# Kernel tuning notes

Hardware: AMD Instinct MI355X
Metric: run time of the kernel (lower is better)

## Reference

```python
import jax, jax.numpy as jnp
import numpy as np


def setup_inputs() -> dict:
    key = jax.random.key(0)
    hidden_states = jax.random.normal(key, (8, 4096, 768), dtype=jnp.float32)
    return {"hidden_states": hidden_states}


def reference(hidden_states) -> jnp.ndarray:
    # fft along seq dim (-2), then along hidden dim (-1), keep real part.
    # Equivalent to a 2D FFT over the last two axes.
    x = hidden_states.astype(jnp.float32)
    out = jnp.fft.fft(jnp.fft.fft(x, axis=-2), axis=-1).real
    return out.astype(hidden_states.dtype)
```

## Files before the change

kernel.cpp:

```cpp
#include <hip/hip_runtime.h>
#include <hip/hip_bf16.h>

#define N1 4096
#define N2 768
#define NCC 384
#define CG 64
#define WS_NEEDED 100663296ull

__device__ __forceinline__ float2 cadd(float2 a, float2 b){ return make_float2(a.x+b.x, a.y+b.y); }
__device__ __forceinline__ float2 csub(float2 a, float2 b){ return make_float2(a.x-b.x, a.y-b.y); }
__device__ __forceinline__ float2 cmul(float2 a, float2 b){ return make_float2(a.x*b.x - a.y*b.y, a.x*b.y + a.y*b.x); }
__device__ __forceinline__ float2 cnegi(float2 a){ return make_float2(a.y, -a.x); }

__device__ __forceinline__ int rev6(int p) {
  int k = 0;
  #pragma unroll
  for (int i = 0; i < 6; ++i) { k = (k << 2) | (p & 3); p >>= 2; }
  return k;
}

__device__ __forceinline__ void fft8(float2 z[8]) {
  const float RH = 0.70710678118654752f;
  float2 u0=cadd(z[0],z[4]), v0=csub(z[0],z[4]);
  float2 u1=cadd(z[1],z[5]), v1=csub(z[1],z[5]);
  float2 u2=cadd(z[2],z[6]), v2=csub(z[2],z[6]);
  float2 u3=cadd(z[3],z[7]), v3=csub(z[3],z[7]);
  v1 = make_float2(RH*(v1.x+v1.y), RH*(v1.y-v1.x));
  v2 = cnegi(v2);
  v3 = make_float2(RH*(v3.y-v3.x), -RH*(v3.x+v3.y));
  float2 a0=cadd(u0,u2), b0=csub(u0,u2);
  float2 a1=cadd(u1,u3), b1=cnegi(csub(u1,u3));
  float2 c0=cadd(v0,v2), d0=csub(v0,v2);
  float2 c1=cadd(v1,v3), d1=cnegi(csub(v1,v3));
  z[0]=cadd(a0,a1); z[4]=csub(a0,a1);
  z[2]=cadd(b0,b1); z[6]=csub(b0,b1);
  z[1]=cadd(c0,c1); z[5]=csub(c0,c1);
  z[3]=cadd(d0,d1); z[7]=csub(d0,d1);
}

__global__ __launch_bounds__(1024) void p1a_kernel(const float* __restrict__ x,
                                                   float2* __restrict__ ws) {
  __shared__ float4 S4[64*65];
  float2* S = reinterpret_cast<float2*>(S4);
  int bid = blockIdx.x;
  int b8  = bid & 7;
  int rem = bid >> 3;
  int cg  = rem / 64;
  int a   = rem % 64;
  const int t = threadIdx.x, l = t & 63, w = t >> 6;

  const float* src = x + (size_t)b8 * N1 * N2 + (size_t)cg * 256;
  #pragma unroll
  for (int j = 0; j < 4; ++j) {
    int r   = 4*w + j;
    int row = a + 64*r;
    float4 v = *reinterpret_cast<const float4*>(src + (size_t)row * N2 + 4*l);
    S4[r*65 + l] = v;
  }
  __syncthreads();

  const int c = t & 127, b0 = t >> 7;
  float2 z[8];
  #pragma unroll
  for (int b1 = 0; b1 < 8; ++b1) z[b1] = S[(8*b1 + b0)*130 + c];
  fft8(z);
  {
    float sn, cs; __sincosf(-6.283185307179586f/64.f * (float)b0, &sn, &cs);
    float2 wstep = make_float2(cs, sn), wcur = wstep;
    #pragma unroll
    for (int j = 1; j < 8; ++j) { z[j] = cmul(z[j], wcur); wcur = cmul(wcur, wstep); }
  }
  __syncthreads();
  #pragma unroll
  for (int j = 0; j < 8; ++j) S[(j*8 + b0)*130 + c] = z[j];
  __syncthreads();

  const int jj = t >> 7;
  #pragma unroll
  for (int b0i = 0; b0i < 8; ++b0i) z[b0i] = S[(jj*8 + b0i)*130 + c];
  fft8(z);
  float2 wc, w8;
  { float sn, cs; __sincosf(-6.283185307179586f/4096.f * (float)(a*jj), &sn, &cs); wc = make_float2(cs, sn); }
  { float sn, cs; __sincosf(-6.283185307179586f/4096.f * (float)(8*a),  &sn, &cs); w8 = make_float2(cs, sn); }
  float2* wdst = ws + ((size_t)b8*64)*64*NCC + (size_t)a*NCC + cg*128 + c;
  #pragma unroll
  for (int m = 0; m < 8; ++m) {
    int kb = 8*m + jj;
    wdst[(size_t)kb * 64 * NCC] = cmul(z[m], wc);
    wc = cmul(wc, w8);
  }
}

__global__ __launch_bounds__(1024) void p1b_kernel(const float2* __restrict__ ws,
                                                   float* __restrict__ out) {
  __shared__ float2 T[2][4096];
  int bid = blockIdx.x;
  int b8  = bid & 7;
  int rem = bid >> 3;
  int cg  = rem / 32, kbt = rem % 32;
  int kb0 = (kbt == 0) ? 0  : kbt;
  int kb1 = (kbt == 0) ? 32 : 64 - kbt;
  const int t = threadIdx.x, l = t & 63, wv = (t >> 6) & 7, ti = t >> 9;
  const int kb = ti ? kb1 : kb0;

  const float2* wsrc = ws + (((size_t)b8*64 + kb)*64)*NCC + cg*CG + l;
  float2 z[8];
  #pragma unroll
  for (int a1 = 0; a1 < 8; ++a1)
    z[a1] = wsrc[(size_t)(8*a1 + wv) * NCC];
  fft8(z);
  float fac = -6.283185307179586f/64.0f * (float)wv;
  #pragma unroll
  for (int q = 1; q < 8; ++q) {
    float sn, cs; __sincosf(fac * (float)q, &sn, &cs);
    z[q] = cmul(z[q], make_float2(cs, sn));
  }
  #pragma unroll
  for (int q = 0; q < 8; ++q) T[ti][(q*8 + wv)*64 + l] = z[q];
  __syncthreads();
  #pragma unroll
  for (int a0 = 0; a0 < 8; ++a0) z[a0] = T[ti][(wv*8 + a0)*64 + l];
  fft8(z);
  __syncthreads();
  #pragma unroll
  for (int ka1 = 0; ka1 < 8; ++ka1) T[ti][(8*ka1 + wv)*64 + l] = z[ka1];
  __syncthreads();

  const size_t obase = (size_t)b8 * N1 * N2;
  #pragma unroll
  for (int it = 0; it < 8; ++it) {
    int ka = 8*it + wv;
    int tj, kap;
    if (kbt == 0) { tj = ti; kap = ti ? (63 - ka) : ((64 - ka) & 63); }
    else          { tj = 1 - ti; kap = 63 - ka; }
    float2 Zk = T[ti][ka*64 + l];
    float2 Zp = T[tj][kap*64 + l];
    int r = kb + 64*ka;
    float2 o;
    if (r <= 2048) o = make_float2(0.5f*(Zk.x + Zp.x), 0.5f*(Zk.y + Zp.y));
    else           o = make_float2(0.5f*(Zp.y - Zk.y), 0.5f*(Zk.x - Zp.x));
    *reinterpret_cast<float2*>(out + obase + (size_t)r * N2 + 2*(cg*CG + l)) = o;
  }
}

#define PADI(i) ((i) + ((i) >> 4))
#define CPBUF 4352

__device__ __forceinline__ void bfly4p(float2* arr, int base, int M, float fac, int np) {
  float2 a0 = arr[PADI(base)], a1 = arr[PADI(base+M)];
  float2 a2 = arr[PADI(base+2*M)], a3 = arr[PADI(base+3*M)];
  float2 t0 = cadd(a0,a2), t1 = csub(a0,a2);
  float2 t2 = cadd(a1,a3), t3 = cnegi(csub(a1,a3));
  float2 y0 = cadd(t0,t2), y1 = cadd(t1,t3), y2 = csub(t0,t2), y3 = csub(t1,t3);
  float ang = fac * (float)np;
  float sn, cs; __sincosf(ang, &sn, &cs);
  float2 w1 = make_float2(cs, sn);
  float2 w2 = cmul(w1,w1);
  float2 w3 = cmul(w2,w1);
  arr[PADI(base)]     = y0;
  arr[PADI(base+M)]   = cmul(y1,w1);
  arr[PADI(base+2*M)] = cmul(y2,w2);
  arr[PADI(base+3*M)] = cmul(y3,w3);
}

__global__ __launch_bounds__(1024) void fft_seq_fused(const float* __restrict__ x,
                                                      float* __restrict__ out) {
  extern __shared__ float2 lds[];
  int bid = blockIdx.x;
  int wg  = (bid & 7) * 96 + (bid >> 3);
  int b   = wg / 96;
  int g   = wg % 96;
  const int t = threadIdx.x;
  const size_t base = (size_t)b * N1 * N2 + 8 * (size_t)g;

  for (int r = t; r < N1; r += 1024) {
    const float* p = x + base + (size_t)r * N2;
    float4 A  = *reinterpret_cast<const float4*>(p);
    float4 Bv = *reinterpret_cast<const float4*>(p + 4);
    int ip = PADI(r);
    lds[ip]             = make_float2(A.x, A.y);
    lds[CPBUF + ip]     = make_float2(A.z, A.w);
    lds[2*CPBUF + ip]   = make_float2(Bv.x, Bv.y);
    lds[3*CPBUF + ip]   = make_float2(Bv.z, Bv.w);
  }
  __syncthreads();

  const int wv  = t >> 6;
  const int cp  = wv & 3;
  const int idx = ((wv >> 2) << 6) + (t & 63);
  float2* buf = lds + cp * CPBUF;

  #pragma unroll
  for (int s = 0; s < 6; ++s) {
    int lm = 10 - 2*s;
    int M  = 1 << lm;
    float fac = -6.283185307179586f / (float)(4*M);
    #pragma unroll
    for (int jj = 0; jj < 4; ++jj) {
      int j   = idx + (jj << 8);
      int np  = j & (M-1);
      int grp = j >> lm;
      int bse = (grp << (lm+2)) + np;
      bfly4p(buf, bse, M, fac, np);
    }
    __syncthreads();
  }

  float* orow = out + base;
  #pragma unroll
  for (int i = 0; i < 4; ++i) {
    int k  = ((t & 63) << 6) + (t >> 6) + (i << 4);
    int km = (N1 - k) & (N1 - 1);
    int pk = PADI(rev6(k));
    int pn = PADI(rev6(km));
    float o[8];
    #pragma unroll
    for (int c = 0; c < 4; ++c) {
      float2 zk = lds[c*CPBUF + pk];
      float2 zn = lds[c*CPBUF + pn];
      if (k <= 2048) { o[2*c] = 0.5f*(zk.x + zn.x); o[2*c+1] = 0.5f*(zk.y + zn.y); }
      else           { o[2*c] = 0.5f*(zn.y - zk.y); o[2*c+1] = 0.5f*(zk.x - zn.x); }
    }
    float* q = orow + (size_t)k * N2;
    *reinterpret_cast<float4*>(q)     = make_float4(o[0], o[1], o[2], o[3]);
    *reinterpret_cast<float4*>(q + 4) = make_float4(o[4], o[5], o[6], o[7]);
  }
}

__global__ __launch_bounds__(256) void fft_hid_kernel(float* __restrict__ out) {
  __shared__ float T[4][12*69];
  const int grp = threadIdx.x >> 6;
  const int l   = threadIdx.x & 63;
  int task = blockIdx.x * 4 + grp;
  int b  = task / 2049;
  int t1 = task - b * 2049;
  const bool special = (t1 == 0) || (t1 == 2048);
  float* baseB = out + (size_t)b * N1 * N2;
  float* pre = baseB + (size_t)t1 * N2;
  float* pim = baseB + (size_t)(N1 - t1) * N2;

  float2 z[12];
  #pragma unroll
  for (int m = 0; m < 12; ++m) {
    float re = pre[(m << 6) + l];
    float im = special ? 0.0f : pim[(m << 6) + l];
    z[m] = make_float2(re, im);
  }

  float2 A[3][4];
  #pragma unroll
  for (int q = 0; q < 3; ++q) {
    float2 s0 = z[q], s1 = z[3+q], s2 = z[6+q], s3 = z[9+q];
    float2 t0 = cadd(s0,s2), t1v = csub(s0,s2);
    float2 t2 = cadd(s1,s3), t3 = cnegi(csub(s1,s3));
    A[q][0] = cadd(t0,t2); A[q][1] = cadd(t1v,t3);
    A[q][2] = csub(t0,t2); A[q][3] = csub(t1v,t3);
  }
  const float h3 = 0.8660254037844386f;
  const float2 W1[4] = { {1.f,0.f}, {h3,-0.5f}, {0.5f,-h3}, {0.f,-1.f} };
  const float2 W2[4] = { {1.f,0.f}, {0.5f,-h3}, {-0.5f,-h3}, {-1.f,0.f} };
  float2 y[12];
  #pragma unroll
  for (int k4 = 0; k4 < 4; ++k4) {
    float2 C0 = A[0][k4];
    float2 C1 = cmul(A[1][k4], W1[k4]);
    float2 C2 = cmul(A[2][k4], W2[k4]);
    float2 tt = cadd(C1,C2), d = csub(C1,C2);
    float2 u  = make_float2(C0.x - 0.5f*tt.x, C0.y - 0.5f*tt.y);
    float2 idd = make_float2(h3*d.y, -h3*d.x);
    y[k4]   = cadd(C0, tt);
    y[k4+4] = cadd(u, idd);
    y[k4+8] = csub(u, idd);
  }

  float base = -6.283185307179586f * (float)l / 768.0f;
  #pragma unroll
  for (int km = 1; km < 12; ++km) {
    float sn, cs; __sincosf(base * (float)km, &sn, &cs);
    y[km] = cmul(y[km], make_float2(cs, sn));
  }

  #pragma unroll
  for (int st = 0; st < 6; ++st) {
    int h = 32 >> st;
    int j = l & (h - 1);
    float sn, cs; __sincosf(-3.14159265358979f * (float)j / (float)h, &sn, &cs);
    float2 w = make_float2(cs, sn);
    bool hi = (l & h) != 0;
    #pragma unroll
    for (int m = 0; m < 12; ++m) {
      float px = __shfl_xor(y[m].x, h, 64);
      float py = __shfl_xor(y[m].y, h, 64);
      float2 p = make_float2(px, py);
      float2 lo  = cadd(y[m], p);
      float2 hiv = cmul(csub(p, y[m]), w);
      y[m] = hi ? hiv : lo;
    }
  }

  int r = ((l&1)<<5)|((l&2)<<3)|((l&4)<<1)|((l&8)>>1)|((l&16)>>3)|((l&32)>>5);
  float* Tb = T[grp];
  #pragma unroll
  for (int km = 0; km < 12; ++km) Tb[km*69 + r] = y[km].x;
  __syncthreads();

  #pragma unroll
  for (int mp = 0; mp < 12; ++mp) {
    int k = (mp << 6) + l;
    float v = Tb[(k % 12)*69 + (k / 12)];
    pre[k] = v;
    if (!special) pim[(N2 - k) % N2] = v;
  }
}

extern "C" void kernel_launch(void* const* d_in, const int* in_sizes, int n_in,
                              void* d_out, int out_size, void* d_ws, size_t ws_size,
                              hipStream_t stream) {
  const float* x = (const float*)d_in[0];
  float* out = (float*)d_out;
  if (ws_size >= WS_NEEDED) {
    float2* ws = (float2*)d_ws;
    p1a_kernel<<<dim3(1536), dim3(1024), 0, stream>>>(x, ws);
    p1b_kernel<<<dim3(1536), dim3(1024), 0, stream>>>(ws, out);
  } else {
    (void)hipFuncSetAttribute(reinterpret_cast<const void*>(&fft_seq_fused),
                              hipFuncAttributeMaxDynamicSharedMemorySize,
                              4 * CPBUF * (int)sizeof(float2));
    fft_seq_fused<<<dim3(768), dim3(1024), 4 * CPBUF * sizeof(float2), stream>>>(x, out);
  }
  fft_hid_kernel<<<dim3(4098), dim3(256), 0, stream>>>(out);
}
```

Measured before the change: 111.0 us.

## Store FFT intermediates in bf16 workspace and read them in hidden-dim pass

The intermediate complex results between the sequence-FFT stages and before the hidden-dim FFT are now packed as bf16 pairs (32-bit per complex) instead of float2. The p1a workspace layout is also reorganised so writes become contiguous blocks, and p1b writes to a second bf16 workspace that a new hidden-dim kernel reads. This roughly halves intermediate global memory traffic. The cost is reduced precision, roughly 3 significant digits, which may exceed output tolerance for large FFT sums.

```diff
diff --git a/kernel.cpp b/kernel.cpp
--- a/kernel.cpp
+++ b/kernel.cpp
@@ -4,13 +4,25 @@
 #define N1 4096
 #define N2 768
 #define NCC 384
-#define CG 64
 #define WS_NEEDED 100663296ull
+#define WS1_UINTS 12582912ull
 
 __device__ __forceinline__ float2 cadd(float2 a, float2 b){ return make_float2(a.x+b.x, a.y+b.y); }
 __device__ __forceinline__ float2 csub(float2 a, float2 b){ return make_float2(a.x-b.x, a.y-b.y); }
 __device__ __forceinline__ float2 cmul(float2 a, float2 b){ return make_float2(a.x*b.x - a.y*b.y, a.x*b.y + a.y*b.x); }
 __device__ __forceinline__ float2 cnegi(float2 a){ return make_float2(a.y, -a.x); }
+
+__device__ __forceinline__ unsigned pack_bf2(float2 v) {
+  unsigned ax = __float_as_uint(v.x); ax = (ax + 0x7FFFu + ((ax >> 16) & 1u)) >> 16;
+  unsigned ay = __float_as_uint(v.y); ay = (ay + 0x7FFFu + ((ay >> 16) & 1u)) & 0xFFFF0000u;
+  return ax | ay;
+}
+__device__ __forceinline__ float2 unpack_bf2(unsigned u) {
+  return make_float2(__uint_as_float(u << 16), __uint_as_float(u & 0xFFFF0000u));
+}
+__device__ __forceinline__ float bf2f(unsigned short u) {
+  return __uint_as_float((unsigned)u << 16);
+}
 
 __device__ __forceinline__ int rev6(int p) {
   int k = 0;
@@ -39,7 +51,7 @@
 }
 
 __global__ __launch_bounds__(1024) void p1a_kernel(const float* __restrict__ x,
-                                                   float2* __restrict__ ws) {
+                                                   unsigned* __restrict__ ws1) {
   __shared__ float4 S4[64*65];
   float2* S = reinterpret_cast<float2*>(S4);
   int bid = blockIdx.x;
@@ -54,8 +66,7 @@
   for (int j = 0; j < 4; ++j) {
     int r   = 4*w + j;
     int row = a + 64*r;
-    float4 v = *reinterpret_cast<const float4*>(src + (size_t)row * N2 + 4*l);
-    S4[r*65 + l] = v;
+    S4[r*65 + l] = *reinterpret_cast<const float4*>(src + (size_t)row * N2 + 4*l);
   }
   __syncthreads();
 
@@ -82,17 +93,16 @@
   float2 wc, w8;
   { float sn, cs; __sincosf(-6.283185307179586f/4096.f * (float)(a*jj), &sn, &cs); wc = make_float2(cs, sn); }
   { float sn, cs; __sincosf(-6.283185307179586f/4096.f * (float)(8*a),  &sn, &cs); w8 = make_float2(cs, sn); }
-  float2* wdst = ws + ((size_t)b8*64)*64*NCC + (size_t)a*NCC + cg*128 + c;
+  unsigned* wdst = ws1 + (((size_t)b8*64 + a)*3 + cg)*8192 + (size_t)jj*128 + c;
   #pragma unroll
   for (int m = 0; m < 8; ++m) {
-    int kb = 8*m + jj;
-    wdst[(size_t)kb * 64 * NCC] = cmul(z[m], wc);
+    wdst[(size_t)m * 1024] = pack_bf2(cmul(z[m], wc));
     wc = cmul(wc, w8);
   }
 }
 
-__global__ __launch_bounds__(1024) void p1b_kernel(const float2* __restrict__ ws,
-                                                   float* __restrict__ out) {
+__global__ __launch_bounds__(1024) void p1b_kernel(const unsigned* __restrict__ ws1,
+                                                   unsigned* __restrict__ ws2) {
   __shared__ float2 T[2][4096];
   int bid = blockIdx.x;
   int b8  = bid & 7;
@@ -102,12 +112,14 @@
   int kb1 = (kbt == 0) ? 32 : 64 - kbt;
   const int t = threadIdx.x, l = t & 63, wv = (t >> 6) & 7, ti = t >> 9;
   const int kb = ti ? kb1 : kb0;
-
-  const float2* wsrc = ws + (((size_t)b8*64 + kb)*64)*NCC + cg*CG + l;
+  const int cgA = cg >> 1, chalf = (cg & 1) * 64;
+
+  const unsigned* wsrc = ws1 + ((size_t)b8*64*3 + cgA)*8192
+                             + (size_t)kb*128 + chalf + l;
   float2 z[8];
   #pragma unroll
   for (int a1 = 0; a1 < 8; ++a1)
-    z[a1] = wsrc[(size_t)(8*a1 + wv) * NCC];
+    z[a1] = unpack_bf2(wsrc[(size_t)(8*a1 + wv) * 24576]);
   fft8(z);
   float fac = -6.283185307179586f/64.0f * (float)wv;
   #pragma unroll
@@ -126,7 +138,7 @@
   for (int ka1 = 0; ka1 < 8; ++ka1) T[ti][(8*ka1 + wv)*64 + l] = z[ka1];
   __syncthreads();
 
-  const size_t obase = (size_t)b8 * N1 * N2;
+  unsigned* wout = ws2 + (size_t)b8 * N1 * NCC + (size_t)cg*64 + l;
   #pragma unroll
   for (int it = 0; it < 8; ++it) {
     int ka = 8*it + wv;
@@ -139,7 +151,96 @@
     float2 o;
     if (r <= 2048) o = make_float2(0.5f*(Zk.x + Zp.x), 0.5f*(Zk.y + Zp.y));
     else           o = make_float2(0.5f*(Zp.y - Zk.y), 0.5f*(Zk.x - Zp.x));
-    *reinterpret_cast<float2*>(out + obase + (size_t)r * N2 + 2*(cg*CG + l)) = o;
+    wout[(size_t)r * NCC] = pack_bf2(o);
+  }
+}
+
+__global__ __launch_bounds__(256) void fft_hid_bf16(const unsigned* __restrict__ ws2,
+                                                    float* __restrict__ out) {
+  __shared__ float T[4][12*69];
+  const int grp = threadIdx.x >> 6;
+  const int l   = threadIdx.x & 63;
+  int task = blockIdx.x * 4 + grp;
+  int b  = task / 2049;
+  int t1 = task - b * 2049;
+  const bool special = (t1 == 0) || (t1 == 2048);
+  const int mrow = special ? t1 : (N1 - t1);
+  const unsigned short* pre16 = (const unsigned short*)ws2 + ((size_t)b*N1 + t1)*N2;
+  const unsigned short* pim16 = (const unsigned short*)ws2 + ((size_t)b*N1 + mrow)*N2;
+
+  float2 z[12];
+  #pragma unroll
+  for (int m = 0; m < 12; ++m) {
+    float re = bf2f(pre16[(m << 6) + l]);
+    float im = special ? 0.0f : bf2f(pim16[(m << 6) + l]);
+    z[m] = make_float2(re, im);
+  }
+
+  float2 A[3][4];
+  #pragma unroll
+  for (int q = 0; q < 3; ++q) {
+    float2 s0 = z[q], s1 = z[3+q], s2 = z[6+q], s3 = z[9+q];
+    float2 t0 = cadd(s0,s2), t1v = csub(s0,s2);
+    float2 t2 = cadd(s1,s3), t3 = cnegi(csub(s1,s3));
+    A[q][0] = cadd(t0,t2); A[q][1] = cadd(t1v,t3);
+    A[q][2] = csub(t0,t2); A[q][3] = csub(t1v,t3);
+  }
+  const float h3 = 0.8660254037844386f;
+  const float2 W1[4] = { {1.f,0.f}, {h3,-0.5f}, {0.5f,-h3}, {0.f,-1.f} };
+  const float2 W2[4] = { {1.f,0.f}, {0.5f,-h3}, {-0.5f,-h3}, {-1.f,0.f} };
+  float2 y[12];
+  #pragma unroll
+  for (int k4 = 0; k4 < 4; ++k4) {
+    float2 C0 = A[0][k4];
+    float2 C1 = cmul(A[1][k4], W1[k4]);
+    float2 C2 = cmul(A[2][k4], W2[k4]);
+    float2 tt = cadd(C1,C2), d = csub(C1,C2);
+    float2 u  = make_float2(C0.x - 0.5f*tt.x, C0.y - 0.5f*tt.y);
+    float2 idd = make_float2(h3*d.y, -h3*d.x);
+    y[k4]   = cadd(C0, tt);
+    y[k4+4] = cadd(u, idd);
+    y[k4+8] = csub(u, idd);
+  }
+
+  float base = -6.283185307179586f * (float)l / 768.0f;
+  #pragma unroll
+  for (int km = 1; km < 12; ++km) {
+    float sn, cs; __sincosf(base * (float)km, &sn, &cs);
+    y[km] = cmul(y[km], make_float2(cs, sn));
+  }
+
+  #pragma unroll
+  for (int st = 0; st < 6; ++st) {
+    int h = 32 >> st;
+    int j = l & (h - 1);
+    float sn, cs; __sincosf(-3.14159265358979f * (float)j / (float)h, &sn, &cs);
+    float2 w = make_float2(cs, sn);
+    bool hi = (l & h) != 0;
+    #pragma unroll
+    for (int m = 0; m < 12; ++m) {
+      float px = __shfl_xor(y[m].x, h, 64);
+      float py = __shfl_xor(y[m].y, h, 64);
+      float2 p = make_float2(px, py);
+      float2 lo  = cadd(y[m], p);
+      float2 hiv = cmul(csub(p, y[m]), w);
+      y[m] = hi ? hiv : lo;
+    }
+  }
+
+  int r = ((l&1)<<5)|((l&2)<<3)|((l&4)<<1)|((l&8)>>1)|((l&16)>>3)|((l&32)>>5);
+  float* Tb = T[grp];
+  #pragma unroll
+  for (int km = 0; km < 12; ++km) Tb[km*69 + r] = y[km].x;
+  __syncthreads();
+
+  float* pre = out + ((size_t)b*N1 + t1)*N2;
+  float* pim = out + ((size_t)b*N1 + mrow)*N2;
+  #pragma unroll
+  for (int mp = 0; mp < 12; ++mp) {
+    int k = (mp << 6) + l;
+    float v = Tb[(k % 12)*69 + (k / 12)];
+    pre[k] = v;
+    if (!special) pim[(N2 - k) % N2] = v;
   }
 }
 
@@ -227,7 +328,7 @@
   }
 }
 
-__global__ __launch_bounds__(256) void fft_hid_kernel(float* __restrict__ out) {
+__global__ __launch_bounds__(256) void fft_hid_f32(float* __restrict__ out) {
   __shared__ float T[4][12*69];
   const int grp = threadIdx.x >> 6;
   const int l   = threadIdx.x & 63;
@@ -235,9 +336,10 @@
   int b  = task / 2049;
   int t1 = task - b * 2049;
   const bool special = (t1 == 0) || (t1 == 2048);
+  const int mrow = special ? t1 : (N1 - t1);
   float* baseB = out + (size_t)b * N1 * N2;
   float* pre = baseB + (size_t)t1 * N2;
-  float* pim = baseB + (size_t)(N1 - t1) * N2;
+  float* pim = baseB + (size_t)mrow * N2;
 
   float2 z[12];
   #pragma unroll
@@ -319,14 +421,16 @@
   const float* x = (const float*)d_in[0];
   float* out = (float*)d_out;
   if (ws_size >= WS_NEEDED) {
-    float2* ws = (float2*)d_ws;
-    p1a_kernel<<<dim3(1536), dim3(1024), 0, stream>>>(x, ws);
-    p1b_kernel<<<dim3(1536), dim3(1024), 0, stream>>>(ws, out);
+    unsigned* ws1 = (unsigned*)d_ws;
+    unsigned* ws2 = ws1 + WS1_UINTS;
+    p1a_kernel<<<dim3(1536), dim3(1024), 0, stream>>>(x, ws1);
+    p1b_kernel<<<dim3(1536), dim3(1024), 0, stream>>>(ws1, ws2);
+    fft_hid_bf16<<<dim3(4098), dim3(256), 0, stream>>>(ws2, out);
   } else {
     (void)hipFuncSetAttribute(reinterpret_cast<const void*>(&fft_seq_fused),
                               hipFuncAttributeMaxDynamicSharedMemorySize,
                               4 * CPBUF * (int)sizeof(float2));
     fft_seq_fused<<<dim3(768), dim3(1024), 4 * CPBUF * sizeof(float2), stream>>>(x, out);
-  }
-  fft_hid_kernel<<<dim3(4098), dim3(256), 0, stream>>>(out);
-}
+    fft_hid_f32<<<dim3(4098), dim3(256), 0, stream>>>(out);
+  }
+}
```

Measured after the change: 94.33 us. -15.0%, faster.
